# Kernel optimization log

Hardware: AMD Instinct MI355X
Metric: run time of the kernel (lower is better)

## Reference

```python
import jax, jax.numpy as jnp
import numpy as np


def squash(s, axis):
    # torch: mag_sq/(1+mag_sq) * s/mag, reduced over the given axis
    mag_sq = jnp.sum(s * s, axis=axis, keepdims=True)
    mag = jnp.sqrt(mag_sq)
    return mag_sq / (1.0 + mag_sq) * (s / mag)


def setup_inputs() -> dict:
    key = jax.random.key(0)
    ks = jax.random.split(key, 13)
    B, D_IN, H = 64, 227989, 512
    NU, CO, K = 8, 8, 8            # num_primary_units, conv out channels, kernel
    L = (H - K) // 2 + 1           # 253
    PSIZE = NU * 0 + CO * L        # 2024 per primary capsule
    NOUT, USIZE = 4, 64            # output capsules
    f32 = jnp.float32
    return {
        "x": jax.random.normal(ks[0], (B, D_IN), f32),
        "fc_w": jax.random.normal(ks[1], (H, D_IN), f32) * 0.002,
        "fc_b": jax.random.normal(ks[2], (H,), f32) * 0.01,
        "conv_w": jax.random.normal(ks[3], (NU, CO, 1, K), f32) * 0.1,
        "conv_b": jax.random.normal(ks[4], (NU, CO), f32) * 0.01,
        "W_dig": jax.random.normal(ks[5], (PSIZE, NOUT, USIZE, NU), f32) * 0.05,
        "fc2_w1": jax.random.normal(ks[6], (128, 256), f32) * 0.05,
        "fc2_b1": jnp.zeros((128,), f32),
        "fc2_w2": jax.random.normal(ks[7], (64, 128), f32) * 0.08,
        "fc2_b2": jnp.zeros((64,), f32),
        "fc2_w3": jax.random.normal(ks[8], (2, 64), f32) * 0.1,
        "fc2_b3": jnp.zeros((2,), f32),
    }


def reference(x, fc_w, fc_b, conv_w, conv_b, W_dig,
              fc2_w1, fc2_b1, fc2_w2, fc2_b2, fc2_w3, fc2_b3):
    B = x.shape[0]
    # fc + ReLU (nn.ReLU overwrote the LeakyReLU attribute)
    sdae = jnp.maximum(x @ fc_w.T + fc_b, 0.0)[:, None, :]   # [B,1,512]

    # primary capsules (no routing): 8 ConvUnits fused into one conv
    NU, CO, _, K = conv_w.shape
    rhs = conv_w.reshape(NU * CO, 1, K)
    u = jax.lax.conv_general_dilated(sdae, rhs, (2,), 'VALID',
                                     dimension_numbers=('NCH', 'OIH', 'NCH'))
    u = u + conv_b.reshape(1, NU * CO, 1)                     # [B,64,253]
    u = u.reshape(B, NU, -1)                                  # [B,8,2024]
    u = squash(u, 2)

    # digits capsule: dynamic routing, 3 iterations
    xt = jnp.swapaxes(u, 1, 2)                                # [B,2024,8]
    u_hat = jnp.einsum('cjdi,bci->bcjd', W_dig, xt)           # [B,2024,4,64]
    C, J = W_dig.shape[0], W_dig.shape[1]
    b_ij = jnp.zeros((C, J), u_hat.dtype)
    for _ in range(3):
        c_ij = jax.nn.softmax(b_ij, axis=0)                   # softmax over in_channels
        s_j = jnp.einsum('cj,bcjd->bjd', c_ij, u_hat)         # [B,4,64]
        v_j = squash(s_j, 1)                                  # torch squashes dim=2 = capsule dim j
        b_ij = b_ij + jnp.mean(jnp.einsum('bcjd,bjd->bcj', u_hat, v_j), axis=0)

    caps = v_j.reshape(B, -1)                                 # [B,256]
    lrelu = lambda z: jnp.where(z >= 0, z, 0.01 * z)          # LeakyReLU; dropout in eval = identity
    h = lrelu(caps @ fc2_w1.T + fc2_b1)
    h = lrelu(h @ fc2_w2.T + fc2_b2)
    logits = h @ fc2_w3.T + fc2_b3                            # [B,2]
    return (logits, sdae)
```

## Files before the change

### kernel.cpp

```cpp
#include <hip/hip_runtime.h>
#include <hip/hip_bf16.h>

typedef __attribute__((ext_vector_type(8))) short s16x8;
typedef __attribute__((ext_vector_type(4))) float f32x4;

#define D_IN 227989
#define KSPLIT 128
#define KC 1792
#define NSTEPS 28
#define APITCH 68
#define BUFSZ (128 * APITCH)

__device__ __forceinline__ s16x8 pk2(f32x4 lo, f32x4 hi) {
    union { int i[4]; s16x8 s; } u;
    asm("v_cvt_pk_bf16_f32 %0, %1, %2" : "=v"(u.i[0]) : "v"(lo[0]), "v"(lo[1]));
    asm("v_cvt_pk_bf16_f32 %0, %1, %2" : "=v"(u.i[1]) : "v"(lo[2]), "v"(lo[3]));
    asm("v_cvt_pk_bf16_f32 %0, %1, %2" : "=v"(u.i[2]) : "v"(hi[0]), "v"(hi[1]));
    asm("v_cvt_pk_bf16_f32 %0, %1, %2" : "=v"(u.i[3]) : "v"(hi[2]), "v"(hi[3]));
    return u.s;
}

__device__ __forceinline__ s16x8 cvt8(const float* p) {
    return pk2(*(const f32x4*)p, *(const f32x4*)(p + 4));
}

__device__ __forceinline__ void gload_lds(const float* g, float* l) {
    __builtin_amdgcn_global_load_lds(
        (const __attribute__((address_space(1))) void*)g,
        (__attribute__((address_space(3))) void*)l, 4, 0, 0);
}

__device__ __forceinline__ void stage_tile(const float* ga, const float* gb,
                                           float* lbase, int wid) {
    float* la = lbase + (wid * 16) * APITCH;
    float* lb = lbase + (64 + wid * 16) * APITCH;
    #pragma unroll
    for (int i = 0; i < 16; ++i) {
        gload_lds(ga + (long)i * D_IN, la + i * APITCH);
        gload_lds(gb + (long)i * D_IN, lb + i * APITCH);
    }
}

__device__ __forceinline__ void compute_tile(const float* buf, int wid,
                                             int frow, int koct, f32x4* acc) {
    const float* B = buf + (64 + wid * 16 + frow) * APITCH + koct * 8;
    const s16x8 b0 = cvt8(B);
    const s16x8 b1 = cvt8(B + 32);
    const float* A = buf + frow * APITCH + koct * 8;
    #pragma unroll
    for (int m = 0; m < 4; ++m) {
        const s16x8 a0 = cvt8(A + m * 16 * APITCH);
        const s16x8 a1 = cvt8(A + m * 16 * APITCH + 32);
        acc[m] = __builtin_amdgcn_mfma_f32_16x16x32_bf16(a0, b0, acc[m], 0, 0, 0);
        acc[m] = __builtin_amdgcn_mfma_f32_16x16x32_bf16(a1, b1, acc[m], 0, 0, 0);
    }
}

__global__ __launch_bounds__(256) void k_fc_gemm(const float* __restrict__ x,
                                                 const float* __restrict__ w,
                                                 float* __restrict__ part) {
    __shared__ __align__(16) float lds[4 * BUFSZ];
    const int t = threadIdx.x;
    const int wid = t >> 6, lane = t & 63;
    const int frow = lane & 15, koct = lane >> 4;
    const int bx = blockIdx.x;
    const int nt = bx & 7, ks = bx >> 3;
    const long k0 = (long)ks * KC;

    const float* ga = x + (long)(wid * 16) * D_IN + k0 + lane;
    const float* gb = w + (long)(nt * 64 + wid * 16) * D_IN + k0 + lane;

    f32x4 acc[4] = {};

    if (k0 + KC <= D_IN) {
        stage_tile(ga, gb, lds + 0 * BUFSZ, wid);
        stage_tile(ga + 64, gb + 64, lds + 1 * BUFSZ, wid);
        #pragma unroll 1
        for (int s = 0; s < NSTEPS; ++s) {
            if (s + 2 < NSTEPS)
                stage_tile(ga + (s + 2) * 64, gb + (s + 2) * 64,
                           lds + ((s + 2) & 3) * BUFSZ, wid);
            if (s + 2 < NSTEPS)      asm volatile("s_waitcnt vmcnt(63)" ::: "memory");
            else if (s + 1 < NSTEPS) asm volatile("s_waitcnt vmcnt(32)" ::: "memory");
            else                     asm volatile("s_waitcnt vmcnt(0)"  ::: "memory");
            __builtin_amdgcn_s_barrier();
            asm volatile("" ::: "memory");
            compute_tile(lds + (s & 3) * BUFSZ, wid, frow, koct, acc);
        }
    } else {
        const int rem = (int)(D_IN - k0);
        const int nst = (rem + 63) >> 6;
        for (int s = 0; s < nst; ++s) {
            const int kk = s * 64 + lane;
            const bool ok = kk < rem;
            float va[16], vb[16];
            #pragma unroll
            for (int i = 0; i < 16; ++i) {
                va[i] = ok ? ga[(long)i * D_IN + s * 64] : 0.0f;
                vb[i] = ok ? gb[(long)i * D_IN + s * 64] : 0.0f;
            }
            __syncthreads();
            #pragma unroll
            for (int i = 0; i < 16; ++i) {
                lds[(wid * 16 + i) * APITCH + lane] = va[i];
                lds[(64 + wid * 16 + i) * APITCH + lane] = vb[i];
            }
            __syncthreads();
            compute_tile(lds, wid, frow, koct, acc);
        }
    }

    const int g16 = nt * 4 + wid;
    float* __restrict__ po = part + ((long)(g16 * KSPLIT + ks) << 10);
    #pragma unroll
    for (int m = 0; m < 4; ++m)
        #pragma unroll
        for (int r = 0; r < 4; ++r)
            po[(m * 16 + koct * 4 + r) * 16 + frow] = acc[m][r];
}

__global__ __launch_bounds__(256) void k_fc_reduce(const float* __restrict__ part,
                                                   const float* __restrict__ bias,
                                                   float* __restrict__ sdae) {
    const int i = blockIdx.x * 256 + threadIdx.x;
    const int m = i >> 9, n = i & 511;
    const int nt = n >> 4, nl = n & 15;
    const float* p = part + ((long)nt * KSPLIT << 10) + m * 16 + nl;
    float s = 0.f;
    #pragma unroll 4
    for (int ks = 0; ks < KSPLIT; ++ks) s += p[(long)ks << 10];
    s += bias[n];
    sdae[i] = fmaxf(s, 0.0f);
}

__global__ __launch_bounds__(256) void k_conv_squash(const float* __restrict__ sdae,
                                                     const float* __restrict__ cw,
                                                     const float* __restrict__ cb,
                                                     float* __restrict__ xt) {
    __shared__ float row_s[512];
    __shared__ float us[64 * 253];
    __shared__ float part[256];
    __shared__ float scale_s[8];
    const int b = blockIdx.x, t = threadIdx.x;
    row_s[t] = sdae[b * 512 + t];
    row_s[t + 256] = sdae[b * 512 + t + 256];
    __syncthreads();
    const int ch = t >> 2, lq = t & 3;
    float wreg[8];
    #pragma unroll
    for (int k = 0; k < 8; ++k) wreg[k] = cw[ch * 8 + k];
    const float bias = cb[ch];
    const int l0 = lq * 64;
    const int l1 = (lq == 3) ? 253 : (l0 + 64);
    float ssq = 0.f;
    for (int l = l0; l < l1; ++l) {
        float v = bias;
        #pragma unroll
        for (int k = 0; k < 8; ++k) v += row_s[2 * l + k] * wreg[k];
        us[ch * 253 + l] = v;
        ssq += v * v;
    }
    part[t] = ssq;
    __syncthreads();
    if (t < 8) {
        float s = 0.f;
        for (int i = 0; i < 32; ++i) s += part[t * 32 + i];
        scale_s[t] = sqrtf(s) / (1.0f + s);
    }
    __syncthreads();
    const int nu = ch >> 3, co = ch & 7;
    const float sc = scale_s[nu];
    for (int l = l0; l < l1; ++l)
        xt[(long)b * 16192 + (long)(co * 253 + l) * 8 + nu] = us[ch * 253 + l] * sc;
}

template <int UNIFORM>
__global__ __launch_bounds__(256) void k_route_s(const float* __restrict__ W,
                                                 const float* __restrict__ xt,
                                                 const float* __restrict__ cij,
                                                 float* __restrict__ spart) {
    __shared__ __align__(16) float xs[64 * 132];
    __shared__ __align__(16) float wsh[16 * 768];
    const int bx = blockIdx.x;
    const int j = bx >> 6, cs = bx & 63;
    const int c0 = cs * 32;
    const int t = threadIdx.x;
    const int bg = t >> 4, dg = t & 15;
    float acc[4][4] = {};
    #pragma unroll 1
    for (int cc0 = 0; cc0 < 32; cc0 += 16) {
        {
            const int bb = t >> 2, p = t & 3;
            const float* src = xt + (long)bb * 16192 + (long)(c0 + cc0) * 8 + p * 32;
            float* dst = &xs[bb * 132 + p * 32];
            if (c0 + cc0 + 16 <= 2024) {
                #pragma unroll
                for (int e = 0; e < 32; e += 4) *(f32x4*)(dst + e) = *(const f32x4*)(src + e);
            } else {
                for (int e = 0; e < 32; ++e) {
                    int cidx = c0 + cc0 + ((p * 32 + e) >> 3);
                    dst[e] = (cidx < 2024) ? src[e] : 0.0f;
                }
            }
        }
        {
            const int ccs = t >> 4, dp = t & 15;
            const int c = c0 + cc0 + ccs;
            float* o = &wsh[ccs * 768 + dp * 48];
            if (c < 2024) {
                const float sc = UNIFORM ? (1.0f / 2024.0f) : cij[j * 2024 + c];
                const float* wsrc = W + (long)c * 2048 + j * 512 + dp * 32;
                #pragma unroll
                for (int dd = 0; dd < 4; ++dd) {
                    f32x4 w0 = *(const f32x4*)(wsrc + dd * 8);
                    f32x4 w1 = *(const f32x4*)(wsrc + dd * 8 + 4);
                    float* od = o + dd * 12;
                    od[0] = w0[0] * sc; od[1] = w0[1] * sc; od[2] = w0[2] * sc; od[3] = w0[3] * sc;
                    od[4] = w1[0] * sc; od[5] = w1[1] * sc; od[6] = w1[2] * sc; od[7] = w1[3] * sc;
                }
            } else {
                #pragma unroll
                for (int dd = 0; dd < 4; ++dd) {
                    float* od = o + dd * 12;
                    #pragma unroll
                    for (int e = 0; e < 8; ++e) od[e] = 0.0f;
                }
            }
        }
        __syncthreads();
        int ccN = 2024 - c0 - cc0;
        if (ccN > 16) ccN = 16;
        for (int cc = 0; cc < ccN; ++cc) {
            float xv[4][8], wv[4][8];
            #pragma unroll
            for (int bb = 0; bb < 4; ++bb) {
                *(f32x4*)&xv[bb][0] = *(const f32x4*)&xs[(bg * 4 + bb) * 132 + cc * 8];
                *(f32x4*)&xv[bb][4] = *(const f32x4*)&xs[(bg * 4 + bb) * 132 + cc * 8 + 4];
            }
            #pragma unroll
            for (int dd = 0; dd < 4; ++dd) {
                const int d = dg + dd * 16;
                *(f32x4*)&wv[dd][0] = *(const f32x4*)&wsh[cc * 768 + d * 12];
                *(f32x4*)&wv[dd][4] = *(const f32x4*)&wsh[cc * 768 + d * 12 + 4];
            }
            #pragma unroll
            for (int bb = 0; bb < 4; ++bb)
                #pragma unroll
                for (int dd = 0; dd < 4; ++dd)
                    #pragma unroll
                    for (int i = 0; i < 8; ++i)
                        acc[bb][dd] += xv[bb][i] * wv[dd][i];
        }
        __syncthreads();
    }
    float* sp = spart + ((long)bx << 12);
    #pragma unroll
    for (int bb = 0; bb < 4; ++bb)
        #pragma unroll
        for (int dd = 0; dd < 4; ++dd)
            sp[(bg * 4 + bb) * 64 + dg + dd * 16] = acc[bb][dd];
}

__global__ __launch_bounds__(256) void k_route_v(const float* __restrict__ spart,
                                                 float* __restrict__ v) {
    __shared__ float sj[256];
    const int b = blockIdx.x, t = threadIdx.x;
    const int d = t & 63;
    const int j = t >> 6;
    float s = 0.f;
    #pragma unroll 4
    for (int cs = 0; cs < 64; ++cs)
        s += spart[((long)(j * 64 + cs) << 12) + (b << 6) + d];
    sj[t] = s;
    __syncthreads();
    float msq = 0.f;
    #pragma unroll
    for (int q = 0; q < 4; ++q) { float z = sj[q * 64 + d]; msq += z * z; }
    v[(b << 8) + t] = s * (sqrtf(msq) / (1.0f + msq));
}

template <int ADD>
__global__ __launch_bounds__(256) void k_route_a(const float* __restrict__ W,
                                                 const float* __restrict__ xt,
                                                 const float* __restrict__ v,
                                                 float* __restrict__ bij) {
    __shared__ __align__(16) float xts[64 * 68];
    __shared__ __align__(16) float vts[4 * 4360];
    __shared__ float red[256];
    const int c0 = blockIdx.x * 8;
    const int t = threadIdx.x;
    for (int idx = t; idx < 16384; idx += 256) {
        int b = idx >> 8, r = idx & 255;
        vts[(r >> 6) * 4360 + (r & 63) * 68 + b] = v[idx];
    }
    for (int idx = t; idx < 4096; idx += 256) {
        int b = idx >> 6, r = idx & 63;
        xts[r * 68 + b] = xt[(long)b * 16192 + (long)c0 * 8 + r];
    }
    __syncthreads();
    const int cc = t >> 5, jj = (t >> 3) & 3, p = t & 7;
    float Wreg[8][8];
    const float* wb = W + (long)(c0 + cc) * 2048 + jj * 512;
    #pragma unroll
    for (int dd = 0; dd < 8; ++dd) {
        const int d = p + dd * 8;
        *(f32x4*)&Wreg[dd][0] = *(const f32x4*)(wb + d * 8);
        *(f32x4*)&Wreg[dd][4] = *(const f32x4*)(wb + d * 8 + 4);
    }
    float a0 = 0.f, a1 = 0.f, a2 = 0.f, a3 = 0.f;
    for (int b0 = 0; b0 < 64; b0 += 4) {
        float xq[8][4];
        #pragma unroll
        for (int i = 0; i < 8; ++i)
            *(f32x4*)&xq[i][0] = *(const f32x4*)&xts[(cc * 8 + i) * 68 + b0];
        #pragma unroll
        for (int dd = 0; dd < 8; ++dd) {
            const int d = p + dd * 8;
            f32x4 vq = *(const f32x4*)&vts[jj * 4360 + d * 68 + b0];
            float u0 = 0, u1 = 0, u2 = 0, u3 = 0;
            #pragma unroll
            for (int i = 0; i < 8; ++i) {
                const float wv = Wreg[dd][i];
                u0 += wv * xq[i][0]; u1 += wv * xq[i][1];
                u2 += wv * xq[i][2]; u3 += wv * xq[i][3];
            }
            a0 += u0 * vq[0]; a1 += u1 * vq[1]; a2 += u2 * vq[2]; a3 += u3 * vq[3];
        }
    }
    red[t] = a0 + a1 + a2 + a3;
    __syncthreads();
    if (p == 0) {
        float s = 0.f;
        #pragma unroll
        for (int q2 = 0; q2 < 8; ++q2) s += red[t + q2];
        s *= (1.0f / 64.0f);
        const int idx = (c0 + cc) * 4 + jj;
        bij[idx] = ADD ? (bij[idx] + s) : s;
    }
}

__global__ __launch_bounds__(256) void k_softmax(const float* __restrict__ bij,
                                                 float* __restrict__ cij) {
    __shared__ float red[256];
    const int j = blockIdx.x, t = threadIdx.x;
    float vals[8];
    float m = -1e30f;
    #pragma unroll
    for (int q = 0; q < 8; ++q) {
        const int c = q * 256 + t;
        const float z = (c < 2024) ? bij[c * 4 + j] : -1e30f;
        vals[q] = z;
        m = fmaxf(m, z);
    }
    red[t] = m;
    __syncthreads();
    for (int s = 128; s > 0; s >>= 1) {
        if (t < s) red[t] = fmaxf(red[t], red[t + s]);
        __syncthreads();
    }
    m = red[0];
    __syncthreads();
    float sum = 0.f;
    #pragma unroll
    for (int q = 0; q < 8; ++q) {
        const int c = q * 256 + t;
        const float e = (c < 2024) ? __expf(vals[q] - m) : 0.0f;
        vals[q] = e;
        sum += e;
    }
    red[t] = sum;
    __syncthreads();
    for (int s = 128; s > 0; s >>= 1) {
        if (t < s) red[t] += red[t + s];
        __syncthreads();
    }
    const float inv = 1.0f / red[0];
    #pragma unroll
    for (int q = 0; q < 8; ++q) {
        const int c = q * 256 + t;
        if (c < 2024) cij[j * 2024 + c] = vals[q] * inv;
    }
}

__global__ __launch_bounds__(256) void k_fc2(const float* __restrict__ v,
                                             const float* __restrict__ w1, const float* __restrict__ b1,
                                             const float* __restrict__ w2, const float* __restrict__ b2,
                                             const float* __restrict__ w3, const float* __restrict__ b3,
                                             float* __restrict__ logits) {
    __shared__ float caps[256], h1[128], h2[64];
    const int b = blockIdx.x, t = threadIdx.x;
    caps[t] = v[b * 256 + t];
    __syncthreads();
    if (t < 128) {
        float s = b1[t];
        const float* wr = w1 + t * 256;
        for (int k = 0; k < 256; ++k) s += wr[k] * caps[k];
        h1[t] = (s >= 0.f) ? s : 0.01f * s;
    }
    __syncthreads();
    if (t < 64) {
        float s = b2[t];
        const float* wr = w2 + t * 128;
        for (int k = 0; k < 128; ++k) s += wr[k] * h1[k];
        h2[t] = (s >= 0.f) ? s : 0.01f * s;
    }
    __syncthreads();
    if (t < 2) {
        float s = b3[t];
        const float* wr = w3 + t * 64;
        for (int k = 0; k < 64; ++k) s += wr[k] * h2[k];
        logits[b * 2 + t] = s;
    }
}

extern "C" void kernel_launch(void* const* d_in, const int* in_sizes, int n_in,
                              void* d_out, int out_size, void* d_ws, size_t ws_size,
                              hipStream_t stream) {
    const float* x      = (const float*)d_in[0];
    const float* fc_w   = (const float*)d_in[1];
    const float* fc_b   = (const float*)d_in[2];
    const float* conv_w = (const float*)d_in[3];
    const float* conv_b = (const float*)d_in[4];
    const float* W_dig  = (const float*)d_in[5];
    const float* w1 = (const float*)d_in[6];
    const float* b1 = (const float*)d_in[7];
    const float* w2 = (const float*)d_in[8];
    const float* b2 = (const float*)d_in[9];
    const float* w3 = (const float*)d_in[10];
    const float* b3 = (const float*)d_in[11];

    float* out    = (float*)d_out;
    float* logits = out;
    float* sdae   = out + 128;

    float* ws     = (float*)d_ws;
    float* ws_fc  = ws;
    float* ws_xt  = ws_fc + 4194304;
    float* ws_sp  = ws_xt + 1036288;
    float* ws_v   = ws_sp + 1048576;
    float* ws_bij = ws_v + 16384;
    float* ws_cij = ws_bij + 8096;

    k_fc_gemm<<<1024, 256, 0, stream>>>(x, fc_w, ws_fc);
    k_fc_reduce<<<128, 256, 0, stream>>>(ws_fc, fc_b, sdae);
    k_conv_squash<<<64, 256, 0, stream>>>(sdae, conv_w, conv_b, ws_xt);

    k_route_s<1><<<256, 256, 0, stream>>>(W_dig, ws_xt, ws_cij, ws_sp);
    k_route_v<<<64, 256, 0, stream>>>(ws_sp, ws_v);
    k_route_a<0><<<253, 256, 0, stream>>>(W_dig, ws_xt, ws_v, ws_bij);
    k_softmax<<<4, 256, 0, stream>>>(ws_bij, ws_cij);
    k_route_s<0><<<256, 256, 0, stream>>>(W_dig, ws_xt, ws_cij, ws_sp);
    k_route_v<<<64, 256, 0, stream>>>(ws_sp, ws_v);
    k_route_a<1><<<253, 256, 0, stream>>>(W_dig, ws_xt, ws_v, ws_bij);
    k_softmax<<<4, 256, 0, stream>>>(ws_bij, ws_cij);
    k_route_s<0><<<256, 256, 0, stream>>>(W_dig, ws_xt, ws_cij, ws_sp);
    k_route_v<<<64, 256, 0, stream>>>(ws_sp, ws_v);

    k_fc2<<<64, 256, 0, stream>>>(ws_v, w1, b1, w2, b2, w3, b3, logits);
}
```

Baseline: 303.9 us.

## Stage FC GEMM tiles with 16-byte global-to-LDS loads and double buffering

Replaces the per-float global_load_lds staging with 16-byte-wide direct-to-LDS loads. Each row starts at an address rounded down to 16 bytes, which shifts it by row&3 elements, so the reads out of LDS use per-lane selects to realign the data before the bf16 conversion. The LDS ring drops from four buffers to two, with explicit barriers and waitcnt on both sides of compute. The aim is to cut the number of load instructions and raise memory throughput on this bandwidth-bound GEMM, at the cost of extra select ALU work, more synchronisation and less prefetch depth. The tail path also gains some dead code and an extra sync.

Result: no change. 305.2 us (+0.4%).

```diff
diff --git a/kernel.cpp b/kernel.cpp
--- a/kernel.cpp
+++ b/kernel.cpp
@@ -8,8 +8,8 @@
 #define KSPLIT 128
 #define KC 1792
 #define NSTEPS 28
-#define APITCH 68
-#define BUFSZ (128 * APITCH)
+#define RPITCH 68
+#define BUFSZ (128 * RPITCH)
 
 __device__ __forceinline__ s16x8 pk2(f32x4 lo, f32x4 hi) {
     union { int i[4]; s16x8 s; } u;
@@ -20,76 +20,111 @@
     return u.s;
 }
 
-__device__ __forceinline__ s16x8 cvt8(const float* p) {
-    return pk2(*(const f32x4*)p, *(const f32x4*)(p + 4));
-}
-
-__device__ __forceinline__ void gload_lds(const float* g, float* l) {
+__device__ __forceinline__ void gload_lds16(const float* g, float* l) {
     __builtin_amdgcn_global_load_lds(
         (const __attribute__((address_space(1))) void*)g,
-        (__attribute__((address_space(3))) void*)l, 4, 0, 0);
-}
-
-__device__ __forceinline__ void stage_tile(const float* ga, const float* gb,
-                                           float* lbase, int wid) {
-    float* la = lbase + (wid * 16) * APITCH;
-    float* lb = lbase + (64 + wid * 16) * APITCH;
-    #pragma unroll
-    for (int i = 0; i < 16; ++i) {
-        gload_lds(ga + (long)i * D_IN, la + i * APITCH);
-        gload_lds(gb + (long)i * D_IN, lb + i * APITCH);
-    }
-}
-
-__device__ __forceinline__ void compute_tile(const float* buf, int wid,
-                                             int frow, int koct, f32x4* acc) {
-    const float* B = buf + (64 + wid * 16 + frow) * APITCH + koct * 8;
-    const s16x8 b0 = cvt8(B);
-    const s16x8 b1 = cvt8(B + 32);
-    const float* A = buf + frow * APITCH + koct * 8;
+        (__attribute__((address_space(3))) void*)l, 16, 0, 0);
+}
+
+__device__ __forceinline__ s16x8 sel8(const float* rowp, int pos0, bool b0, bool b1) {
+    f32x4 i0 = *(const f32x4*)(rowp + pos0);
+    f32x4 i1 = *(const f32x4*)(rowp + pos0 + 4);
+    f32x4 i2 = *(const f32x4*)(rowp + pos0 + 8);
+    float in[12] = {i0[0], i0[1], i0[2], i0[3], i1[0], i1[1], i1[2], i1[3],
+                    i2[0], i2[1], i2[2], i2[3]};
+    float tv[10];
+    #pragma unroll
+    for (int i = 0; i < 10; ++i) tv[i] = b0 ? in[i + 1] : in[i];
+    f32x4 lo, hi;
+    #pragma unroll
+    for (int e = 0; e < 4; ++e) lo[e] = b1 ? tv[e + 2] : tv[e];
+    #pragma unroll
+    for (int e = 0; e < 4; ++e) hi[e] = b1 ? tv[e + 6] : tv[e + 4];
+    return pk2(lo, hi);
+}
+
+__device__ __forceinline__ void compute_tile(const float* buf, int wid, int frow,
+                                             int koct, bool b0, bool b1, f32x4* acc) {
+    const float* B = buf + (64 + wid * 16 + frow) * RPITCH;
+    const s16x8 bb0 = sel8(B, koct * 8, b0, b1);
+    const s16x8 bb1 = sel8(B, 32 + koct * 8, b0, b1);
     #pragma unroll
     for (int m = 0; m < 4; ++m) {
-        const s16x8 a0 = cvt8(A + m * 16 * APITCH);
-        const s16x8 a1 = cvt8(A + m * 16 * APITCH + 32);
-        acc[m] = __builtin_amdgcn_mfma_f32_16x16x32_bf16(a0, b0, acc[m], 0, 0, 0);
-        acc[m] = __builtin_amdgcn_mfma_f32_16x16x32_bf16(a1, b1, acc[m], 0, 0, 0);
+        const float* A = buf + (m * 16 + frow) * RPITCH;
+        const s16x8 a0 = sel8(A, koct * 8, b0, b1);
+        const s16x8 a1 = sel8(A, 32 + koct * 8, b0, b1);
+        acc[m] = __builtin_amdgcn_mfma_f32_16x16x32_bf16(a0, bb0, acc[m], 0, 0, 0);
+        acc[m] = __builtin_amdgcn_mfma_f32_16x16x32_bf16(a1, bb1, acc[m], 0, 0, 0);
     }
 }
 
 __global__ __launch_bounds__(256) void k_fc_gemm(const float* __restrict__ x,
                                                  const float* __restrict__ w,
                                                  float* __restrict__ part) {
-    __shared__ __align__(16) float lds[4 * BUFSZ];
+    __shared__ __align__(16) float lds[2 * BUFSZ];
     const int t = threadIdx.x;
     const int wid = t >> 6, lane = t & 63;
     const int frow = lane & 15, koct = lane >> 4;
     const int bx = blockIdx.x;
     const int nt = bx & 7, ks = bx >> 3;
     const long k0 = (long)ks * KC;
-
-    const float* ga = x + (long)(wid * 16) * D_IN + k0 + lane;
-    const float* gb = w + (long)(nt * 64 + wid * 16) * D_IN + k0 + lane;
+    const bool b0 = (frow & 1) != 0, b1 = (frow & 2) != 0;
 
     f32x4 acc[4] = {};
 
-    if (k0 + KC <= D_IN) {
-        stage_tile(ga, gb, lds + 0 * BUFSZ, wid);
-        stage_tile(ga + 64, gb + 64, lds + 1 * BUFSZ, wid);
+    if (ks < KSPLIT - 1) {
+        const float* gp[9];
+        int jdst[9];
+        #pragma unroll
+        for (int jj = 0; jj < 9; ++jj) {
+            int j = jj * 4 + wid;
+            if (j >= 34) j -= 34;
+            jdst[jj] = j * 256;
+            const int ch = j * 64 + lane;
+            const int row = ch / 17;
+            const int c = ch - row * 17;
+            const float* base = (row < 64)
+                ? (x + (long)row * D_IN)
+                : (w + (long)(nt * 64 + (row - 64)) * D_IN);
+            gp[jj] = base + (k0 - (row & 3)) + c * 4;
+        }
+        float* L0 = lds;
+        float* L1 = lds + BUFSZ;
+
+#define STAGE(BUF, OFF) do {                                   \
+    _Pragma("unroll")                                          \
+    for (int jj = 0; jj < 9; ++jj)                             \
+        gload_lds16(gp[jj] + (OFF), (BUF) + jdst[jj]);         \
+} while (0)
+
+        STAGE(L0, 0);
         #pragma unroll 1
-        for (int s = 0; s < NSTEPS; ++s) {
-            if (s + 2 < NSTEPS)
-                stage_tile(ga + (s + 2) * 64, gb + (s + 2) * 64,
-                           lds + ((s + 2) & 3) * BUFSZ, wid);
-            if (s + 2 < NSTEPS)      asm volatile("s_waitcnt vmcnt(63)" ::: "memory");
-            else if (s + 1 < NSTEPS) asm volatile("s_waitcnt vmcnt(32)" ::: "memory");
-            else                     asm volatile("s_waitcnt vmcnt(0)"  ::: "memory");
+        for (int s = 0; s < NSTEPS; s += 2) {
+            STAGE(L1, (s + 1) * 64);
+            asm volatile("s_waitcnt vmcnt(9)" ::: "memory");
             __builtin_amdgcn_s_barrier();
             asm volatile("" ::: "memory");
-            compute_tile(lds + (s & 3) * BUFSZ, wid, frow, koct, acc);
-        }
+            compute_tile(L0, wid, frow, koct, b0, b1, acc);
+            asm volatile("s_waitcnt lgkmcnt(0)" ::: "memory");
+            __builtin_amdgcn_s_barrier();
+            if (s + 2 < NSTEPS) {
+                STAGE(L0, (s + 2) * 64);
+                asm volatile("s_waitcnt vmcnt(9)" ::: "memory");
+            } else {
+                asm volatile("s_waitcnt vmcnt(0)" ::: "memory");
+            }
+            __builtin_amdgcn_s_barrier();
+            asm volatile("" ::: "memory");
+            compute_tile(L1, wid, frow, koct, b0, b1, acc);
+            asm volatile("s_waitcnt lgkmcnt(0)" ::: "memory");
+            __builtin_amdgcn_s_barrier();
+        }
+#undef STAGE
     } else {
         const int rem = (int)(D_IN - k0);
         const int nst = (rem + 63) >> 6;
+        const float* ga = x + (long)(wid * 16) * D_IN + k0 + lane;
+        const float* gb = w + (long)(nt * 64 + wid * 16) * D_IN + k0 + lane;
         for (int s = 0; s < nst; ++s) {
             const int kk = s * 64 + lane;
             const bool ok = kk < rem;
@@ -102,11 +137,16 @@
             __syncthreads();
             #pragma unroll
             for (int i = 0; i < 16; ++i) {
-                lds[(wid * 16 + i) * APITCH + lane] = va[i];
-                lds[(64 + wid * 16 + i) * APITCH + lane] = vb[i];
+                lds[(wid * 16 + i) * RPITCH + lane] = va[i];
+                lds[(64 + wid * 16 + i) * RPITCH + lane] = vb[i];
+            }
+            if (lane < 8) {
+                const int rr = (lane & 3), half = lane >> 2;
+                (void)rr; (void)half;
             }
             __syncthreads();
-            compute_tile(lds, wid, frow, koct, acc);
+            compute_tile(lds, wid, frow, koct, false, false, acc);
+            __syncthreads();
         }
     }
 
```
